# Optimization experiments

Measured on AMD Instinct MI355X. Metric: run time of the kernel, lower is better.

Reference implementation:

```python
import jax, jax.numpy as jnp
import numpy as np
import math

# ---- static configuration (mirrors init_kwargs) ----
NQ = 8            # n_qubits (main register)
NA = 2            # n_ancilla = ceil(log2(n_select))
NSEL = 4          # n_select
DEG = 3           # degree
LAYERS = 2        # n_ansatz_layers
KLOC = 2          # k_local
LATENT = 128
B = 256
NROTS = 4 * NQ * LAYERS          # 64
GROUPS = [(s, s + 1) for s in range(NQ - KLOC + 1)]  # sliding 2-local -> 7 groups
NOBS = len(GROUPS)
KDIM = 2 ** KLOC                  # 4
C64 = jnp.complex64
TWO_PI = 2.0 * math.pi

CNOT = jnp.array([[1, 0, 0, 0], [0, 1, 0, 0], [0, 0, 0, 1], [0, 0, 1, 0]], dtype=C64)

# ---- gate matrices (theta may be traced) ----
def ry_mat(th):
    c = jnp.cos(th / 2).astype(C64); s = jnp.sin(th / 2).astype(C64)
    return jnp.stack([jnp.stack([c, -s]), jnp.stack([s, c])])

def rz_mat(th):
    return jnp.diag(jnp.stack([jnp.exp(-0.5j * th), jnp.exp(0.5j * th)])).astype(C64)

def crx_mat(th):
    c = jnp.cos(th / 2).astype(C64); isn = (-1j * jnp.sin(th / 2)).astype(C64)
    one = jnp.ones((), C64)
    m = jnp.zeros((4, 4), C64)
    m = m.at[0, 0].set(one).at[1, 1].set(one)
    m = m.at[2, 2].set(c).at[3, 3].set(c).at[2, 3].set(isn).at[3, 2].set(isn)
    return m

# ---- state-vector gate application (state: (2,)*rank, wire = axis) ----
def apply_1q(state, U, w):
    return jnp.moveaxis(jnp.tensordot(U, state, axes=((1,), (w,))), 0, w)

def apply_2q(state, U, w0, w1):
    st = jnp.tensordot(U.reshape(2, 2, 2, 2), state, axes=((2, 3), (w0, w1)))
    return jnp.moveaxis(st, (0, 1), (w0, w1))

def _sim14_ops(nq, layers):
    ops, idx = [], 0
    for _ in range(layers):
        for i in range(nq):
            ops.append(("ry", (i,), idx)); idx += 1
        for i in range(nq - 1, -1, -1):
            ops.append(("crx", (i, (i + 1) % nq), idx)); idx += 1
        for i in range(nq):
            ops.append(("ry", (i,), idx)); idx += 1
        for i in [nq - 1] + list(range(nq - 1)):
            ops.append(("crx", (i, (i - 1) % nq), idx)); idx += 1
    return ops

def apply_sim14(state, p, layers, adjoint=False):
    ops = _sim14_ops(NQ, layers)
    seq = list(reversed(ops)) if adjoint else ops
    sgn = -1.0 if adjoint else 1.0
    for kind, ws, idx in seq:
        th = sgn * p[idx]
        if kind == "ry":
            state = apply_1q(state, ry_mat(th), ws[0])
        else:
            state = apply_2q(state, crx_mat(th), ws[0], ws[1])
    return state

def pcphase(state, phi):
    # e^{+i phi} on ancilla=|0..0> subspace (first 2^NQ states in (anc, main) ordering), e^{-i phi} elsewhere
    sr = state.reshape(2 ** NQ, 2 ** NA)
    ph = jnp.where(jnp.arange(2 ** NA) == 0, jnp.exp(1j * phi), jnp.exp(-1j * phi)).astype(C64)
    return (sr * ph[None, :]).reshape(state.shape)

def prepare(state, prep_p, adjoint=False):
    if not adjoint:
        for ly in range(NA):          # n_prep_layers == n_ancilla
            for qi in range(NA):
                state = apply_1q(state, ry_mat(prep_p[ly, qi, 0]), NQ + qi)
                state = apply_1q(state, rz_mat(prep_p[ly, qi, 1]), NQ + qi)
            for i in range(NA - 1):
                state = apply_2q(state, CNOT, NQ + i, NQ + i + 1)
    else:
        for ly in reversed(range(NA)):
            for i in reversed(range(NA - 1)):
                state = apply_2q(state, CNOT, NQ + i, NQ + i + 1)
            for qi in reversed(range(NA)):
                state = apply_1q(state, rz_mat(-prep_p[ly, qi, 1]), NQ + qi)
                state = apply_1q(state, ry_mat(-prep_p[ly, qi, 0]), NQ + qi)
    return state

def select(state, ts, adjoint=False):
    # ancilla wires (NQ, NQ+1) are the trailing axes; flattened index == control value s
    sr = state.reshape((2,) * NQ + (2 ** NA,))
    for s in range(NSEL):
        sub = apply_sim14(sr[..., s], ts[s], LAYERS, adjoint=adjoint)
        sr = sr.at[..., s].set(sub)
    return sr.reshape(state.shape)

def create_hermitian(A, Bp, D, N):
    h = jnp.zeros((N, N), C64)
    count = 0
    for i in range(1, N):
        h = h.at[i - 1, i - 1].set(D[i].astype(C64))
        for j in range(i):
            h = h.at[i, j].set((A[count + j] + 1j * Bp[count + j]).astype(C64))
        count += i
    return h + h.conj().T

def simulate(ts, prep_p, sig, qff, H_all):
    # ts: (NSEL, NROTS) for one batch element
    state = jnp.zeros((2,) * (NQ + NA), C64).at[(0,) * (NQ + NA)].set(1.0)
    state = pcphase(state, sig[0])
    for k in range(DEG):
        state = prepare(state, prep_p)
        state = select(state, ts, adjoint=(k % 2 == 1))
        state = prepare(state, prep_p, adjoint=True)
        state = pcphase(state, sig[k + 1])
    state = apply_sim14(state, qff, 1)
    es = []
    for w, (a, b) in enumerate(GROUPS):
        hpsi = apply_2q(state, H_all[w], a, b)
        es.append(jnp.real(jnp.vdot(state, hpsi)))
    return jnp.stack(es).astype(jnp.float32)  # (NOBS,)

def linear(x, w, b):
    return x @ w.T + b

def sinusoidal_embedding(t, dim):
    half = dim // 2
    freqs = jnp.exp(-math.log(10000.0) * jnp.arange(half, dtype=jnp.float32) / half)
    args = t[:, None] * freqs[None]
    return jnp.concatenate([jnp.cos(args), jnp.sin(args)], axis=-1)

def _forward(z_t, t, te_w1, te_b1, te_w2, te_b2, ip_w1, ip_b1, ip_w2, ip_b2,
             prep_params, signal_angles, qff_params, A_obs, B_obs, D_obs, head_w, head_b):
    t_emb = sinusoidal_embedding(t, LATENT)
    t_emb = linear(jax.nn.silu(linear(t_emb, te_w1, te_b1)), te_w2, te_b2)
    h = jnp.concatenate([z_t, t_emb], axis=-1)
    h = linear(jax.nn.silu(linear(h, ip_w1, ip_b1)), ip_w2, ip_b2)
    ts = jax.nn.sigmoid(h).reshape(z_t.shape[0], NSEL, NROTS) * TWO_PI
    H_all = jax.vmap(lambda a, b, d: create_hermitian(a, b, d, KDIM))(A_obs, B_obs, D_obs)  # (NOBS,4,4)
    expvals = jax.vmap(simulate, in_axes=(0, None, None, None, None))(
        ts, prep_params, signal_angles, qff_params, H_all)  # (B, NOBS)
    return linear(expvals, head_w, head_b)  # (B, LATENT)

def setup_inputs() -> dict:
    key = jax.random.key(0)
    ks = jax.random.split(key, 16)
    def n(k, shape, s=0.05):
        return s * jax.random.normal(k, shape, jnp.float32)
    return {
        "z_t": jax.random.normal(ks[0], (B, LATENT), jnp.float32),
        "t": jax.random.uniform(ks[1], (B,), jnp.float32),
        "te_w1": n(ks[2], (LATENT, LATENT)), "te_b1": jnp.zeros((LATENT,), jnp.float32),
        "te_w2": n(ks[3], (LATENT, LATENT)), "te_b2": jnp.zeros((LATENT,), jnp.float32),
        "ip_w1": n(ks[4], (2 * LATENT, 2 * LATENT)), "ip_b1": jnp.zeros((2 * LATENT,), jnp.float32),
        "ip_w2": n(ks[5], (NSEL * NROTS, 2 * LATENT)), "ip_b2": jnp.zeros((NSEL * NROTS,), jnp.float32),
        "prep_params": 0.1 * jax.random.normal(ks[6], (NA, NA, 2), jnp.float32),
        "signal_angles": 0.1 * jax.random.normal(ks[7], (DEG + 1,), jnp.float32),
        "qff_params": jax.random.uniform(ks[8], (4 * NQ,), jnp.float32),
        "A_obs": 2.0 * jax.random.normal(ks[9], (NOBS, KDIM * (KDIM - 1) // 2), jnp.float32),
        "B_obs": 2.0 * jax.random.normal(ks[10], (NOBS, KDIM * (KDIM - 1) // 2), jnp.float32),
        "D_obs": 2.0 * jax.random.normal(ks[11], (NOBS, KDIM), jnp.float32),
        "head_w": n(ks[12], (LATENT, NOBS)), "head_b": jnp.zeros((LATENT,), jnp.float32),
    }

def reference(z_t, t, te_w1, te_b1, te_w2, te_b2, ip_w1, ip_b1, ip_w2, ip_b2,
              prep_params, signal_angles, qff_params, A_obs, B_obs, D_obs, head_w, head_b):
    return _forward(z_t, t, te_w1, te_b1, te_w2, te_b2, ip_w1, ip_b1, ip_w2, ip_b2,
                    prep_params, signal_angles, qff_params, A_obs, B_obs, D_obs, head_w, head_b)
```

## Files before the change

### kernel.cpp

```cpp
#include <hip/hip_runtime.h>
#include <math.h>

#define NOBS 7
#define PI_F 3.14159265358979f


template<int LM>
__device__ __forceinline__ float lane_partner(float x) {
  if constexpr (LM == 1) {
    return __int_as_float(__builtin_amdgcn_mov_dpp(__float_as_int(x), 0xB1, 0xF, 0xF, true));
  } else if constexpr (LM == 2) {
    return __int_as_float(__builtin_amdgcn_mov_dpp(__float_as_int(x), 0x4E, 0xF, 0xF, true));
  } else if constexpr (LM == 4) {
    int a = __builtin_amdgcn_mov_dpp(__float_as_int(x), 0x1B, 0xF, 0xF, true);
    return __int_as_float(__builtin_amdgcn_mov_dpp(a, 0x141, 0xF, 0xF, true));
  } else if constexpr (LM == 8) {
    int a = __builtin_amdgcn_mov_dpp(__float_as_int(x), 0x141, 0xF, 0xF, true);
    return __int_as_float(__builtin_amdgcn_mov_dpp(a, 0x140, 0xF, 0xF, true));
  } else if constexpr (LM == 16) {
#if __has_builtin(__builtin_amdgcn_permlane16_swap)
    unsigned xu = __float_as_uint(x);
    auto r = __builtin_amdgcn_permlane16_swap(xu, xu, false, false);
    return (__uint_as_float(r[0]) + __uint_as_float(r[1])) - x;
#else
// ... 35 lines not shown

__device__ __forceinline__ float rdlane(float v, int idx) {
  return __int_as_float(__builtin_amdgcn_readlane(__float_as_int(v), idx));
}

__device__ __forceinline__ float2 cmul(float2 a, float2 b) {
  return make_float2(a.x*b.x - a.y*b.y, a.x*b.y + a.y*b.x);
}
__device__ __forceinline__ float2 cmulc(float2 a, float2 b) {
  return make_float2(a.x*b.x + a.y*b.y, a.y*b.x - a.x*b.y);
}
__device__ __forceinline__ float2 cadd(float2 a, float2 b) {
  return make_float2(a.x + b.x, a.y + b.y);
}

struct Ctx {
  float4* xw;
  int pp;
  int wv, lane, h;
};

__device__ __forceinline__ float4 wexch(Ctx& cx, const float* vr, const float* vi) {
  float4* buf = cx.xw + cx.pp * 512;
  buf[cx.wv * 64 + cx.lane] = make_float4(vr[0], vr[1], vi[0], vi[1]);
  __syncthreads();
  float4 p = buf[(cx.wv ^ 4) * 64 + cx.lane];
  cx.pp ^= 1;
  return p;
}


template<int W>
__device__ __forceinline__ void ry_lane(float* vr, float* vi, Ctx& cx,
                                        float ct, float st, int idx, float sg) {
  float c = rdlane(ct, idx), s = sg * rdlane(st, idx);
  constexpr int LM = 1 << (5 - W);
  const float ls = (cx.lane & LM) ? s : -s;
#pragma unroll
  for (int r = 0; r < 2; ++r) {
    float pr = lane_partner<LM>(vr[r]);
    float pi = lane_partner<LM>(vi[r]);
    vr[r] = c*vr[r] + ls*pr;
    vi[r] = c*vi[r] + ls*pi;
  }
}

__device__ __forceinline__ void ry_wave6(float* vr, float* vi, Ctx& cx,
                                         float ct, float st, int idx, float sg) {
  float c = rdlane(ct, idx), s = sg * rdlane(st, idx);
  float4 P = wexch(cx, vr, vi);
  const float ls = cx.h ? s : -s;
  vr[0] = c*vr[0] + ls*P.x;  vr[1] = c*vr[1] + ls*P.y;
  vi[0] = c*vi[0] + ls*P.z;  vi[1] = c*vi[1] + ls*P.w;
}

__device__ __forceinline__ void ry_reg7(float* vr, float* vi,
                                        float ct, float st, int idx, float sg) {
  float c = rdlane(ct, idx), s = sg * rdlane(st, idx);
  float a0 = vr[0], a1 = vr[1];
  vr[0] = c*a0 - s*a1;  vr[1] = s*a0 + c*a1;
  float b0 = vi[0], b1 = vi[1];
  vi[0] = c*b0 - s*b1;  vi[1] = s*b0 + c*b1;
}

template<int C, int T>
__device__ __forceinline__ void crx_ll(float* vr, float* vi, Ctx& cx,
                                       float ct, float st, int idx, float sg) {
  float c = rdlane(ct, idx), s = sg * rdlane(st, idx);
  constexpr int LC = 1 << (5 - C), LT = 1 << (5 - T);
  const bool act = (cx.lane & LC) != 0;
  const float cp = act ? c : 1.f, sp = act ? s : 0.f;
#pragma unroll
  for (int r = 0; r < 2; ++r) {
    float pr = lane_partner<LT>(vr[r]);
    float pi = lane_partner<LT>(vi[r]);
    vr[r] = cp*vr[r] + sp*pi;
    vi[r] = cp*vi[r] - sp*pr;
  }
}

template<int T>
__device__ __forceinline__ void crx_7l(float* vr, float* vi, Ctx& cx,
                                       float ct, float st, int idx, float sg) {
  float c = rdlane(ct, idx), s = sg * rdlane(st, idx);
  constexpr int LT = 1 << (5 - T);
  float pr = lane_partner<LT>(vr[1]);
  float pi = lane_partner<LT>(vi[1]);
  vr[1] = c*vr[1] + s*pi;
  vi[1] = c*vi[1] - s*pr;
}

template<int C>
__device__ __forceinline__ void crx_l7(float* vr, float* vi, Ctx& cx,
                                       float ct, float st, int idx, float sg) {
  float c = rdlane(ct, idx), s = sg * rdlane(st, idx);
  constexpr int LC = 1 << (5 - C);
  const bool act = (cx.lane & LC) != 0;
  const float cp = act ? c : 1.f, sp = act ? s : 0.f;
  float xr = vr[0], xi = vi[0], yr = vr[1], yi = vi[1];
  vr[0] = cp*xr + sp*yi;  vi[0] = cp*xi - sp*yr;
  vr[1] = cp*yr + sp*xi;  vi[1] = cp*yi - sp*xr;
}

template<int C>
__device__ __forceinline__ void crx_l6(float* vr, float* vi, Ctx& cx,
                                       float ct, float st, int idx, float sg) {
  float c = rdlane(ct, idx), s = sg * rdlane(st, idx);
  float4 P = wexch(cx, vr, vi);
  constexpr int LC = 1 << (5 - C);
  const bool act = (cx.lane & LC) != 0;
  const float cp = act ? c : 1.f, sp = act ? s : 0.f;
  vr[0] = cp*vr[0] + sp*P.z;  vi[0] = cp*vi[0] - sp*P.x;
  vr[1] = cp*vr[1] + sp*P.w;  vi[1] = cp*vi[1] - sp*P.y;
}

__device__ __forceinline__ void crx_76(float* vr, float* vi, Ctx& cx,
                                       float ct, float st, int idx, float sg) {
  float c = rdlane(ct, idx), s = sg * rdlane(st, idx);
  float4 P = wexch(cx, vr, vi);
  vr[1] = c*vr[1] + s*P.w;
  vi[1] = c*vi[1] - s*P.y;
}

__device__ __forceinline__ void crx_67(float* vr, float* vi, Ctx& cx,
                                       float ct, float st, int idx, float sg) {
  if (cx.h) {
    float c = rdlane(ct, idx), s = sg * rdlane(st, idx);
    float xr = vr[0], xi = vi[0], yr = vr[1], yi = vi[1];
    vr[0] = c*xr + s*yi;  vi[0] = c*xi - s*yr;
    vr[1] = c*yr + s*xi;  vi[1] = c*yi - s*xr;
  }
}

template<int T>
__device__ __forceinline__ void crx_6l(float* vr, float* vi, Ctx& cx,
                                       float ct, float st, int idx, float sg) {
  if (cx.h) {
    float c = rdlane(ct, idx), s = sg * rdlane(st, idx);
    constexpr int LT = 1 << (5 - T);
#pragma unroll
    for (int r = 0; r < 2; ++r) {
      float pr = lane_partner<LT>(vr[r]);
      float pi = lane_partner<LT>(vi[r]);
      vr[r] = c*vr[r] + s*pi;
      vi[r] = c*vi[r] - s*pr;
    }
  }
}


__device__ __forceinline__ void sim14_fwd(float* vr, float* vi, Ctx& cx,
                                          float ct, float st, int off, float sg) {
  ry_lane<0>(vr,vi,cx,ct,st,off+0,sg); ry_lane<1>(vr,vi,cx,ct,st,off+1,sg);
  ry_lane<2>(vr,vi,cx,ct,st,off+2,sg); ry_lane<3>(vr,vi,cx,ct,st,off+3,sg);
  ry_lane<4>(vr,vi,cx,ct,st,off+4,sg); ry_lane<5>(vr,vi,cx,ct,st,off+5,sg);
  ry_wave6(vr,vi,cx,ct,st,off+6,sg);   ry_reg7(vr,vi,ct,st,off+7,sg);
  crx_7l<0>(vr,vi,cx,ct,st,off+8,sg);  crx_67(vr,vi,cx,ct,st,off+9,sg);
  crx_l6<5>(vr,vi,cx,ct,st,off+10,sg); crx_ll<4,5>(vr,vi,cx,ct,st,off+11,sg);
  crx_ll<3,4>(vr,vi,cx,ct,st,off+12,sg); crx_ll<2,3>(vr,vi,cx,ct,st,off+13,sg);
  crx_ll<1,2>(vr,vi,cx,ct,st,off+14,sg); crx_ll<0,1>(vr,vi,cx,ct,st,off+15,sg);
  ry_lane<0>(vr,vi,cx,ct,st,off+16,sg); ry_lane<1>(vr,vi,cx,ct,st,off+17,sg);
  ry_lane<2>(vr,vi,cx,ct,st,off+18,sg); ry_lane<3>(vr,vi,cx,ct,st,off+19,sg);
  ry_lane<4>(vr,vi,cx,ct,st,off+20,sg); ry_lane<5>(vr,vi,cx,ct,st,off+21,sg);
  ry_wave6(vr,vi,cx,ct,st,off+22,sg);   ry_reg7(vr,vi,ct,st,off+23,sg);
  crx_76(vr,vi,cx,ct,st,off+24,sg);     crx_l7<0>(vr,vi,cx,ct,st,off+25,sg);
  crx_ll<1,0>(vr,vi,cx,ct,st,off+26,sg); crx_ll<2,1>(vr,vi,cx,ct,st,off+27,sg);
  crx_ll<3,2>(vr,vi,cx,ct,st,off+28,sg); crx_ll<4,3>(vr,vi,cx,ct,st,off+29,sg);
  crx_ll<5,4>(vr,vi,cx,ct,st,off+30,sg); crx_6l<5>(vr,vi,cx,ct,st,off+31,sg);
}

__device__ __forceinline__ void sim14_adj(float* vr, float* vi, Ctx& cx,
                                          float ct, float st, int off) {
  const float sg = -1.f;
  crx_6l<5>(vr,vi,cx,ct,st,off+31,sg); crx_ll<5,4>(vr,vi,cx,ct,st,off+30,sg);
  crx_ll<4,3>(vr,vi,cx,ct,st,off+29,sg); crx_ll<3,2>(vr,vi,cx,ct,st,off+28,sg);
  crx_ll<2,1>(vr,vi,cx,ct,st,off+27,sg); crx_ll<1,0>(vr,vi,cx,ct,st,off+26,sg);
  crx_l7<0>(vr,vi,cx,ct,st,off+25,sg);   crx_76(vr,vi,cx,ct,st,off+24,sg);
  ry_reg7(vr,vi,ct,st,off+23,sg);        ry_wave6(vr,vi,cx,ct,st,off+22,sg);
  ry_lane<5>(vr,vi,cx,ct,st,off+21,sg); ry_lane<4>(vr,vi,cx,ct,st,off+20,sg);
  ry_lane<3>(vr,vi,cx,ct,st,off+19,sg); ry_lane<2>(vr,vi,cx,ct,st,off+18,sg);
  ry_lane<1>(vr,vi,cx,ct,st,off+17,sg); ry_lane<0>(vr,vi,cx,ct,st,off+16,sg);
  crx_ll<0,1>(vr,vi,cx,ct,st,off+15,sg); crx_ll<1,2>(vr,vi,cx,ct,st,off+14,sg);
  crx_ll<2,3>(vr,vi,cx,ct,st,off+13,sg); crx_ll<3,4>(vr,vi,cx,ct,st,off+12,sg);
  crx_ll<4,5>(vr,vi,cx,ct,st,off+11,sg); crx_l6<5>(vr,vi,cx,ct,st,off+10,sg);
  crx_67(vr,vi,cx,ct,st,off+9,sg);       crx_7l<0>(vr,vi,cx,ct,st,off+8,sg);
  ry_reg7(vr,vi,ct,st,off+7,sg);         ry_wave6(vr,vi,cx,ct,st,off+6,sg);
  ry_lane<5>(vr,vi,cx,ct,st,off+5,sg); ry_lane<4>(vr,vi,cx,ct,st,off+4,sg);
  ry_lane<3>(vr,vi,cx,ct,st,off+3,sg); ry_lane<2>(vr,vi,cx,ct,st,off+2,sg);
  ry_lane<1>(vr,vi,cx,ct,st,off+1,sg); ry_lane<0>(vr,vi,cx,ct,st,off+0,sg);
}


template<int IN, int NP, int MODE>
__device__ __forceinline__ void mlp_layer(const float* __restrict__ W,
    const float* __restrict__ bias, const float* xl, float* yl,
    int rbase, int lane)
{
  const int sub = lane & 7;
  const int g   = lane >> 3;
#pragma unroll
  for (int p = 0; p < NP; ++p) {
    const int row = rbase + p * 8 + g;
    const float4* w4 = (const float4*)(W + row * IN) + sub;
    const float4* x4 = (const float4*)xl + sub;
// ... 17 lines not shown
        float sn, cn;
        __sincosf(th, &sn, &cn);
        ((float2*)yl)[row] = make_float2(cn, sn);
      }
    }
  }
}


__global__ __launch_bounds__(512) void qsvt_kernel(
    const float* __restrict__ z_t, const float* __restrict__ t,
    const float* __restrict__ te_w1, const float* __restrict__ te_b1,
    const float* __restrict__ te_w2, const float* __restrict__ te_b2,
    const float* __restrict__ ip_w1, const float* __restrict__ ip_b1,
    const float* __restrict__ ip_w2, const float* __restrict__ ip_b2,
    const float* __restrict__ prep_p, const float* __restrict__ sig,
    const float* __restrict__ qff, const float* __restrict__ A_obs,
    const float* __restrict__ B_obs, const float* __restrict__ D_obs,
    const float* __restrict__ head_w, const float* __restrict__ head_b,
    float* __restrict__ out)
{
  __shared__ __align__(16) float emb[128];
  __shared__ __align__(16) float y1[128];
  __shared__ __align__(16) float hbuf[256];
  __shared__ __align__(16) float h1[256];
  __shared__ __align__(16) float2 seltab[256];
  __shared__ __align__(16) float2 qtab[32];
  __shared__ __align__(16) float4 xw[2 * 8 * 64];
  __shared__ __align__(16) float2 xanc[128 * 9];
  __shared__ __align__(16) float dumpR[4][256];
  __shared__ __align__(16) float dumpI[4][256];
  __shared__ float redbuf[NOBS][4];
  __shared__ float hdc[NOBS][3], hxc[NOBS][6], hyc[NOBS][6];
  __shared__ __align__(16) float shw[128 * NOBS];
  __shared__ __align__(16) float shb[128];

  const int tid  = threadIdx.x;
  const int lane = tid & 63;
  const int wv   = tid >> 6;
  const int s    = wv & 3;
  const int h    = wv >> 2;
  const int b    = blockIdx.x;

  if (tid < 128) {
    int j = tid & 63;
    float fr = __expf(-9.210340371976184f * (float)j / 64.f);
    float arg = t[b] * fr;
    float sn, cn;
    __sincosf(arg, &sn, &cn);
    emb[tid] = (tid < 64) ? cn : sn;
  } else if (tid < 160) {
    int j = tid - 128;
    float sn, cn;
    __sincosf(0.5f * qff[j], &sn, &cn);
    qtab[j] = make_float2(cn, sn);
  }
  __syncthreads();

  mlp_layer<128, 2, 0>(te_w1, te_b1, emb, y1, wv * 16, lane);
  if (tid < 128) hbuf[tid] = z_t[b * 128 + tid];
  __syncthreads();

  mlp_layer<128, 2, 1>(te_w2, te_b2, y1, hbuf + 128, wv * 16, lane);
  __syncthreads();

  mlp_layer<256, 4, 0>(ip_w1, ip_b1, hbuf, h1, wv * 32, lane);
  __syncthreads();

  mlp_layer<256, 4, 2>(ip_w2, ip_b2, h1, (float*)seltab, wv * 32, lane);

  if (tid < NOBS * 6)      { hxc[tid/6][tid%6] = A_obs[tid]; hyc[tid/6][tid%6] = B_obs[tid]; }
  else if (tid >= 64 && tid < 64 + NOBS*3) { int q = tid - 64; hdc[q/3][q%3] = 2.f * D_obs[(q/3)*4 + (q%3) + 1]; }
#pragma unroll
  for (int i = tid; i < 128*NOBS; i += 512) shw[i] = head_w[i];
  if (tid < 128) shb[tid] = head_b[tid];

  float2 Ga[2][2][2], Gb[2][2][2];
#pragma unroll
  for (int ly = 0; ly < 2; ++ly) {
#pragma unroll
    for (int qi = 0; qi < 2; ++qi) {
      float y = prep_p[ly*4 + qi*2 + 0], z = prep_p[ly*4 + qi*2 + 1];
      float cy, sy, cz, sz;
      __sincosf(0.5f*y, &sy, &cy);
      __sincosf(0.5f*z, &sz, &cz);
      float2 g00 = make_float2( cy*cz, -cy*sz);
      float2 g01 = make_float2(-sy*cz,  sy*sz);
      float2 g10 = make_float2( sy*cz,  sy*sz);
      float2 g11 = make_float2( cy*cz,  cy*sz);
      if (qi == 0) { Ga[ly][0][0]=g00; Ga[ly][0][1]=g01; Ga[ly][1][0]=g10; Ga[ly][1][1]=g11; }
      else         { Gb[ly][0][0]=g00; Gb[ly][0][1]=g01; Gb[ly][1][0]=g10; Gb[ly][1][1]=g11; }
    }
  }
  float2 M[2][4][4];
#pragma unroll
  for (int ly = 0; ly < 2; ++ly) {
    float2 T[4][4];
#pragma unroll
    for (int i = 0; i < 4; ++i)
#pragma unroll
      for (int j = 0; j < 4; ++j)
        T[i][j] = cmul(Ga[ly][i>>1][j>>1], Gb[ly][i&1][j&1]);
#pragma unroll
    for (int j = 0; j < 4; ++j) {
      M[ly][0][j] = T[0][j]; M[ly][1][j] = T[1][j];
      M[ly][2][j] = T[3][j]; M[ly][3][j] = T[2][j];
    }
  }
  float2 U[4][4];
#pragma unroll
  for (int i = 0; i < 4; ++i)
#pragma unroll
    for (int j = 0; j < 4; ++j) {
      float2 acc = make_float2(0.f, 0.f);
#pragma unroll
      for (int kk = 0; kk < 4; ++kk) acc = cadd(acc, cmul(M[1][i][kk], M[0][kk][j]));
      U[i][j] = acc;
    }
  float2 Urow[4], Ucol[4];
#pragma unroll
  for (int j = 0; j < 4; ++j) {
    Urow[j] = s==0 ? U[0][j] : s==1 ? U[1][j] : s==2 ? U[2][j] : U[3][j];
    Ucol[j] = s==0 ? U[j][0] : s==1 ? U[j][1] : s==2 ? U[j][2] : U[j][3];
  }
  float sg0 = sig[0], sg1 = sig[1], sg2 = sig[2], sg3 = sig[3];
  float c1, s1v, c2, s2v, c3, s3v;
  __sincosf(sg1, &s1v, &c1);
  __sincosf(sg2, &s2v, &c2);
  __sincosf(sg3, &s3v, &c3);
  float2 R1[4], R2[4], RF[4];
  {
    float s3s = (s == 0) ? s3v : -s3v;
    float2 d3 = make_float2(c3, s3s);
#pragma unroll
    for (int sp = 0; sp < 4; ++sp) {
      float2 a1 = make_float2(0.f, 0.f), a2 = make_float2(0.f, 0.f);
#pragma unroll
      for (int j = 0; j < 4; ++j) {
        float2 uspj = sp==0 ? U[0][j] : sp==1 ? U[1][j] : sp==2 ? U[2][j] : U[3][j];
        float2 tt = cmulc(Urow[j], uspj);
        float sj = (j == 0) ? 1.f : -1.f;
        a1 = cadd(a1, cmul(tt, make_float2(c1, sj*s1v)));
        a2 = cadd(a2, cmul(tt, make_float2(c2, sj*s2v)));
      }
      R1[sp] = a1; R2[sp] = a2;
      RF[sp] = cmul(d3, make_float2(Ucol[sp].x, -Ucol[sp].y));
    }
  }
  __syncthreads();

  float2 mycs = seltab[(s << 6) | lane];
  float selc = mycs.x, sels = mycs.y;
  float2 myq = qtab[lane & 31];
  float qc = myq.x, qs = myq.y;

  Ctx cx; cx.xw = xw; cx.pp = 0; cx.wv = wv; cx.lane = lane; cx.h = h;

  float vr[2], vi[2];
  vr[0] = 0.f; vr[1] = 0.f; vi[0] = 0.f; vi[1] = 0.f;
  if (lane == 0 && h == 0) {
    float s0n, c0n;
    __sincosf(sg0, &s0n, &c0n);
    float2 a0 = cmul(Urow[0], make_float2(c0n, s0n));
    vr[0] = a0.x; vi[0] = a0.y;
  }

  const int ancbase = (h * 64 + lane) * 9;

  sim14_fwd(vr, vi, cx, selc, sels, 0, 1.f);
  sim14_fwd(vr, vi, cx, selc, sels, 32, 1.f);
  {
#pragma unroll
    for (int r = 0; r < 2; ++r) xanc[ancbase + r*4 + s] = make_float2(vr[r], vi[r]);
    __syncthreads();
#pragma unroll
    for (int r = 0; r < 2; ++r) {
      const float2* p = &xanc[ancbase + r*4];
      float2 o = cmul(R1[0], p[0]);
      o = cadd(o, cmul(R1[1], p[1]));
      o = cadd(o, cmul(R1[2], p[2]));
      o = cadd(o, cmul(R1[3], p[3]));
      vr[r] = o.x; vi[r] = o.y;
    }
    __syncthreads();
  }
  sim14_adj(vr, vi, cx, selc, sels, 32);
  sim14_adj(vr, vi, cx, selc, sels, 0);
  {
#pragma unroll
    for (int r = 0; r < 2; ++r) xanc[ancbase + r*4 + s] = make_float2(vr[r], vi[r]);
    __syncthreads();
#pragma unroll
    for (int r = 0; r < 2; ++r) {
      const float2* p = &xanc[ancbase + r*4];
      float2 o = cmul(R2[0], p[0]);
      o = cadd(o, cmul(R2[1], p[1]));
      o = cadd(o, cmul(R2[2], p[2]));
      o = cadd(o, cmul(R2[3], p[3]));
      vr[r] = o.x; vi[r] = o.y;
    }
    __syncthreads();
  }
  sim14_fwd(vr, vi, cx, selc, sels, 0, 1.f);
  sim14_fwd(vr, vi, cx, selc, sels, 32, 1.f);
  {
#pragma unroll
    for (int r = 0; r < 2; ++r) xanc[ancbase + r*4 + s] = make_float2(vr[r], vi[r]);
    __syncthreads();
#pragma unroll
    for (int r = 0; r < 2; ++r) {
      const float2* p = &xanc[ancbase + r*4];
      float2 o = cmul(RF[0], p[0]);
      o = cadd(o, cmul(RF[1], p[1]));
      o = cadd(o, cmul(RF[2], p[2]));
      o = cadd(o, cmul(RF[3], p[3]));
      vr[r] = o.x; vi[r] = o.y;
    }
    __syncthreads();
  }
  sim14_fwd(vr, vi, cx, qc, qs, 0, 1.f);

  *(float2*)&dumpR[s][(lane << 2) | (h << 1)] = make_float2(vr[0], vr[1]);
  *(float2*)&dumpI[s][(lane << 2) | (h << 1)] = make_float2(vi[0], vi[1]);
  __syncthreads();

  const int w0 = h ? 4 : 0, w1 = h ? NOBS : 4;
  for (int w = w0; w < w1; ++w) {
    const int pb = 6 - w;
    int g = lane;
    int ib = ((g >> pb) << (pb + 2)) | (g & ((1 << pb) - 1));
    float xr[4], xi[4];
#pragma unroll
    for (int i = 0; i < 4; ++i) { xr[i] = dumpR[s][ib + (i << pb)]; xi[i] = dumpI[s][ib + (i << pb)]; }
    float a = hdc[w][0] * (xr[0]*xr[0] + xi[0]*xi[0])
            + hdc[w][1] * (xr[1]*xr[1] + xi[1]*xi[1])
            + hdc[w][2] * (xr[2]*xr[2] + xi[2]*xi[2]);
    const int oi[6] = {1, 2, 2, 3, 3, 3};
    const int oj[6] = {0, 0, 1, 0, 1, 2};
// ... 16 lines not shown

  if (tid < 128) {
    float acc = shb[tid];
#pragma unroll
    for (int w = 0; w < NOBS; ++w) {
      float ev = redbuf[w][0] + redbuf[w][1] + redbuf[w][2] + redbuf[w][3];
      acc += ev * shw[tid*NOBS + w];
    }
    out[b * 128 + tid] = acc;
  }
}

extern "C" void kernel_launch(void* const* d_in, const int* in_sizes, int n_in,
                              void* d_out, int out_size, void* d_ws, size_t ws_size,
                              hipStream_t stream) {
  (void)n_in; (void)out_size; (void)d_ws; (void)ws_size;
  const float* z_t    = (const float*)d_in[0];
  const float* t      = (const float*)d_in[1];
  const float* te_w1  = (const float*)d_in[2];
  const float* te_b1  = (const float*)d_in[3];
  const float* te_w2  = (const float*)d_in[4];
  const float* te_b2  = (const float*)d_in[5];
  const float* ip_w1  = (const float*)d_in[6];
  const float* ip_b1  = (const float*)d_in[7];
  const float* ip_w2  = (const float*)d_in[8];
  const float* ip_b2  = (const float*)d_in[9];
  const float* prep_p = (const float*)d_in[10];
  const float* sig    = (const float*)d_in[11];
  const float* qff    = (const float*)d_in[12];
  const float* A_obs  = (const float*)d_in[13];
  const float* B_obs  = (const float*)d_in[14];
  const float* D_obs  = (const float*)d_in[15];
  const float* head_w = (const float*)d_in[16];
  const float* head_b = (const float*)d_in[17];
  float* out = (float*)d_out;

  int B = in_sizes[1];
  qsvt_kernel<<<B, 512, 0, stream>>>(
      z_t, t, te_w1, te_b1, te_w2, te_b2, ip_w1, ip_b1, ip_w2, ip_b2,
      prep_p, sig, qff, A_obs, B_obs, D_obs, head_w, head_b, out);
}
```

Baseline: 127.2 us.

## Precompute batch-invariant QSVT tables in setup kernel and outline sim14 circuits

Adds a one-block setup kernel that computes the ancilla prep unitary, the signal-rotation reflection matrices, the QFF cos/sin table and the timestep frequency table once, instead of redoing them in every block. The main kernel reads these from workspace and drops the per-thread register arrays R1/R2/RF. The sim14 forward and adjoint circuits become noinline functions with a dynamic shared exchange buffer, which shrinks code size and register pressure. The cost is a second kernel launch plus real function calls and global reads of the tables.

```diff
diff --git a/kernel.cpp b/kernel.cpp
--- a/kernel.cpp
+++ b/kernel.cpp
@@ -73,28 +73,24 @@
   return make_float2(a.x + b.x, a.y + b.y);
 }
 
-struct Ctx {
-  float4* xw;
-  int pp;
-  int wv, lane, h;
-};
-
-__device__ __forceinline__ float4 wexch(Ctx& cx, const float* vr, const float* vi) {
-  float4* buf = cx.xw + cx.pp * 512;
-  buf[cx.wv * 64 + cx.lane] = make_float4(vr[0], vr[1], vi[0], vi[1]);
-  __syncthreads();
-  float4 p = buf[(cx.wv ^ 4) * 64 + cx.lane];
-  cx.pp ^= 1;
-  return p;
+struct S4 { float r0, r1, i0, i1; };
+
+__device__ __forceinline__ float4 wexch(int pp, int wv, int lane,
+                                        const float* vr, const float* vi) {
+  extern __shared__ float4 dxw[];
+  float4* buf = dxw + pp * 512;
+  buf[wv * 64 + lane] = make_float4(vr[0], vr[1], vi[0], vi[1]);
+  __syncthreads();
+  return buf[(wv ^ 4) * 64 + lane];
 }
 
 
 template<int W>
-__device__ __forceinline__ void ry_lane(float* vr, float* vi, Ctx& cx,
-                                        float ct, float st, int idx, float sg) {
+__device__ __forceinline__ void ry_lane_g(float* vr, float* vi, int lane,
+                                          float ct, float st, int idx, float sg) {
   float c = rdlane(ct, idx), s = sg * rdlane(st, idx);
   constexpr int LM = 1 << (5 - W);
-  const float ls = (cx.lane & LM) ? s : -s;
+  const float ls = (lane & LM) ? s : -s;
 #pragma unroll
   for (int r = 0; r < 2; ++r) {
     float pr = lane_partner<LM>(vr[r]);
@@ -104,17 +100,17 @@
   }
 }
 
-__device__ __forceinline__ void ry_wave6(float* vr, float* vi, Ctx& cx,
-                                         float ct, float st, int idx, float sg) {
-  float c = rdlane(ct, idx), s = sg * rdlane(st, idx);
-  float4 P = wexch(cx, vr, vi);
-  const float ls = cx.h ? s : -s;
+__device__ __forceinline__ void ry_wave6_g(float* vr, float* vi, int wv, int lane, int h,
+                                           float ct, float st, int idx, float sg, int pp) {
+  float c = rdlane(ct, idx), s = sg * rdlane(st, idx);
+  float4 P = wexch(pp, wv, lane, vr, vi);
+  const float ls = h ? s : -s;
   vr[0] = c*vr[0] + ls*P.x;  vr[1] = c*vr[1] + ls*P.y;
   vi[0] = c*vi[0] + ls*P.z;  vi[1] = c*vi[1] + ls*P.w;
 }
 
-__device__ __forceinline__ void ry_reg7(float* vr, float* vi,
-                                        float ct, float st, int idx, float sg) {
+__device__ __forceinline__ void ry_reg7_g(float* vr, float* vi,
+                                          float ct, float st, int idx, float sg) {
   float c = rdlane(ct, idx), s = sg * rdlane(st, idx);
   float a0 = vr[0], a1 = vr[1];
   vr[0] = c*a0 - s*a1;  vr[1] = s*a0 + c*a1;
@@ -123,11 +119,11 @@
 }
 
 template<int C, int T>
-__device__ __forceinline__ void crx_ll(float* vr, float* vi, Ctx& cx,
-                                       float ct, float st, int idx, float sg) {
+__device__ __forceinline__ void crx_ll_g(float* vr, float* vi, int lane,
+                                         float ct, float st, int idx, float sg) {
   float c = rdlane(ct, idx), s = sg * rdlane(st, idx);
   constexpr int LC = 1 << (5 - C), LT = 1 << (5 - T);
-  const bool act = (cx.lane & LC) != 0;
+  const bool act = (lane & LC) != 0;
   const float cp = act ? c : 1.f, sp = act ? s : 0.f;
 #pragma unroll
   for (int r = 0; r < 2; ++r) {
@@ -139,8 +135,8 @@
 }
 
 template<int T>
-__device__ __forceinline__ void crx_7l(float* vr, float* vi, Ctx& cx,
-                                       float ct, float st, int idx, float sg) {
+__device__ __forceinline__ void crx_7l_g(float* vr, float* vi,
+                                         float ct, float st, int idx, float sg) {
   float c = rdlane(ct, idx), s = sg * rdlane(st, idx);
   constexpr int LT = 1 << (5 - T);
   float pr = lane_partner<LT>(vr[1]);
@@ -150,11 +146,11 @@
 }
 
 template<int C>
-__device__ __forceinline__ void crx_l7(float* vr, float* vi, Ctx& cx,
-                                       float ct, float st, int idx, float sg) {
+__device__ __forceinline__ void crx_l7_g(float* vr, float* vi, int lane,
+                                         float ct, float st, int idx, float sg) {
   float c = rdlane(ct, idx), s = sg * rdlane(st, idx);
   constexpr int LC = 1 << (5 - C);
-  const bool act = (cx.lane & LC) != 0;
+  const bool act = (lane & LC) != 0;
   const float cp = act ? c : 1.f, sp = act ? s : 0.f;
   float xr = vr[0], xi = vi[0], yr = vr[1], yi = vi[1];
   vr[0] = cp*xr + sp*yi;  vi[0] = cp*xi - sp*yr;
@@ -162,28 +158,28 @@
 }
 
 template<int C>
-__device__ __forceinline__ void crx_l6(float* vr, float* vi, Ctx& cx,
-                                       float ct, float st, int idx, float sg) {
-  float c = rdlane(ct, idx), s = sg * rdlane(st, idx);
-  float4 P = wexch(cx, vr, vi);
+__device__ __forceinline__ void crx_l6_g(float* vr, float* vi, int wv, int lane,
+                                         float ct, float st, int idx, float sg, int pp) {
+  float c = rdlane(ct, idx), s = sg * rdlane(st, idx);
+  float4 P = wexch(pp, wv, lane, vr, vi);
   constexpr int LC = 1 << (5 - C);
-  const bool act = (cx.lane & LC) != 0;
+  const bool act = (lane & LC) != 0;
   const float cp = act ? c : 1.f, sp = act ? s : 0.f;
   vr[0] = cp*vr[0] + sp*P.z;  vi[0] = cp*vi[0] - sp*P.x;
   vr[1] = cp*vr[1] + sp*P.w;  vi[1] = cp*vi[1] - sp*P.y;
 }
 
-__device__ __forceinline__ void crx_76(float* vr, float* vi, Ctx& cx,
-                                       float ct, float st, int idx, float sg) {
-  float c = rdlane(ct, idx), s = sg * rdlane(st, idx);
-  float4 P = wexch(cx, vr, vi);
+__device__ __forceinline__ void crx_76_g(float* vr, float* vi, int wv, int lane,
+                                         float ct, float st, int idx, float sg, int pp) {
+  float c = rdlane(ct, idx), s = sg * rdlane(st, idx);
+  float4 P = wexch(pp, wv, lane, vr, vi);
   vr[1] = c*vr[1] + s*P.w;
   vi[1] = c*vi[1] - s*P.y;
 }
 
-__device__ __forceinline__ void crx_67(float* vr, float* vi, Ctx& cx,
-                                       float ct, float st, int idx, float sg) {
-  if (cx.h) {
+__device__ __forceinline__ void crx_67_g(float* vr, float* vi, int h,
+                                         float ct, float st, int idx, float sg) {
+  if (h) {
     float c = rdlane(ct, idx), s = sg * rdlane(st, idx);
     float xr = vr[0], xi = vi[0], yr = vr[1], yi = vi[1];
     vr[0] = c*xr + s*yi;  vi[0] = c*xi - s*yr;
@@ -192,9 +188,9 @@
 }
 
 template<int T>
-__device__ __forceinline__ void crx_6l(float* vr, float* vi, Ctx& cx,
-                                       float ct, float st, int idx, float sg) {
-  if (cx.h) {
+__device__ __forceinline__ void crx_6l_g(float* vr, float* vi, int h,
+                                         float ct, float st, int idx, float sg) {
+  if (h) {
     float c = rdlane(ct, idx), s = sg * rdlane(st, idx);
     constexpr int LT = 1 << (5 - T);
 #pragma unroll
@@ -208,45 +204,133 @@
 }
 
 
-__device__ __forceinline__ void sim14_fwd(float* vr, float* vi, Ctx& cx,
-                                          float ct, float st, int off, float sg) {
-  ry_lane<0>(vr,vi,cx,ct,st,off+0,sg); ry_lane<1>(vr,vi,cx,ct,st,off+1,sg);
-  ry_lane<2>(vr,vi,cx,ct,st,off+2,sg); ry_lane<3>(vr,vi,cx,ct,st,off+3,sg);
-  ry_lane<4>(vr,vi,cx,ct,st,off+4,sg); ry_lane<5>(vr,vi,cx,ct,st,off+5,sg);
-  ry_wave6(vr,vi,cx,ct,st,off+6,sg);   ry_reg7(vr,vi,ct,st,off+7,sg);
-  crx_7l<0>(vr,vi,cx,ct,st,off+8,sg);  crx_67(vr,vi,cx,ct,st,off+9,sg);
-  crx_l6<5>(vr,vi,cx,ct,st,off+10,sg); crx_ll<4,5>(vr,vi,cx,ct,st,off+11,sg);
-  crx_ll<3,4>(vr,vi,cx,ct,st,off+12,sg); crx_ll<2,3>(vr,vi,cx,ct,st,off+13,sg);
-  crx_ll<1,2>(vr,vi,cx,ct,st,off+14,sg); crx_ll<0,1>(vr,vi,cx,ct,st,off+15,sg);
-  ry_lane<0>(vr,vi,cx,ct,st,off+16,sg); ry_lane<1>(vr,vi,cx,ct,st,off+17,sg);
-  ry_lane<2>(vr,vi,cx,ct,st,off+18,sg); ry_lane<3>(vr,vi,cx,ct,st,off+19,sg);
-  ry_lane<4>(vr,vi,cx,ct,st,off+20,sg); ry_lane<5>(vr,vi,cx,ct,st,off+21,sg);
-  ry_wave6(vr,vi,cx,ct,st,off+22,sg);   ry_reg7(vr,vi,ct,st,off+23,sg);
-  crx_76(vr,vi,cx,ct,st,off+24,sg);     crx_l7<0>(vr,vi,cx,ct,st,off+25,sg);
-  crx_ll<1,0>(vr,vi,cx,ct,st,off+26,sg); crx_ll<2,1>(vr,vi,cx,ct,st,off+27,sg);
-  crx_ll<3,2>(vr,vi,cx,ct,st,off+28,sg); crx_ll<4,3>(vr,vi,cx,ct,st,off+29,sg);
-  crx_ll<5,4>(vr,vi,cx,ct,st,off+30,sg); crx_6l<5>(vr,vi,cx,ct,st,off+31,sg);
-}
-
-__device__ __forceinline__ void sim14_adj(float* vr, float* vi, Ctx& cx,
-                                          float ct, float st, int off) {
+__device__ __noinline__ S4 sim14_fwd(S4 v, float ct, float st, int off) {
+  const int tid = threadIdx.x;
+  const int lane = tid & 63, wv = tid >> 6, h = wv >> 2;
+  float vr[2] = {v.r0, v.r1}, vi[2] = {v.i0, v.i1};
+  const float sg = 1.f;
+  ry_lane_g<0>(vr,vi,lane,ct,st,off+0,sg); ry_lane_g<1>(vr,vi,lane,ct,st,off+1,sg);
+  ry_lane_g<2>(vr,vi,lane,ct,st,off+2,sg); ry_lane_g<3>(vr,vi,lane,ct,st,off+3,sg);
+  ry_lane_g<4>(vr,vi,lane,ct,st,off+4,sg); ry_lane_g<5>(vr,vi,lane,ct,st,off+5,sg);
+  ry_wave6_g(vr,vi,wv,lane,h,ct,st,off+6,sg,0);
+  ry_reg7_g(vr,vi,ct,st,off+7,sg);
+  crx_7l_g<0>(vr,vi,ct,st,off+8,sg);
+  crx_67_g(vr,vi,h,ct,st,off+9,sg);
+  crx_l6_g<5>(vr,vi,wv,lane,ct,st,off+10,sg,1);
+  crx_ll_g<4,5>(vr,vi,lane,ct,st,off+11,sg); crx_ll_g<3,4>(vr,vi,lane,ct,st,off+12,sg);
+  crx_ll_g<2,3>(vr,vi,lane,ct,st,off+13,sg); crx_ll_g<1,2>(vr,vi,lane,ct,st,off+14,sg);
+  crx_ll_g<0,1>(vr,vi,lane,ct,st,off+15,sg);
+  ry_lane_g<0>(vr,vi,lane,ct,st,off+16,sg); ry_lane_g<1>(vr,vi,lane,ct,st,off+17,sg);
+  ry_lane_g<2>(vr,vi,lane,ct,st,off+18,sg); ry_lane_g<3>(vr,vi,lane,ct,st,off+19,sg);
+  ry_lane_g<4>(vr,vi,lane,ct,st,off+20,sg); ry_lane_g<5>(vr,vi,lane,ct,st,off+21,sg);
+  ry_wave6_g(vr,vi,wv,lane,h,ct,st,off+22,sg,0);
+  ry_reg7_g(vr,vi,ct,st,off+23,sg);
+  crx_76_g(vr,vi,wv,lane,ct,st,off+24,sg,1);
+  crx_l7_g<0>(vr,vi,lane,ct,st,off+25,sg);
+  crx_ll_g<1,0>(vr,vi,lane,ct,st,off+26,sg); crx_ll_g<2,1>(vr,vi,lane,ct,st,off+27,sg);
+  crx_ll_g<3,2>(vr,vi,lane,ct,st,off+28,sg); crx_ll_g<4,3>(vr,vi,lane,ct,st,off+29,sg);
+  crx_ll_g<5,4>(vr,vi,lane,ct,st,off+30,sg);
+  crx_6l_g<5>(vr,vi,h,ct,st,off+31,sg);
+  return {vr[0], vr[1], vi[0], vi[1]};
+}
+
+__device__ __noinline__ S4 sim14_adj(S4 v, float ct, float st, int off) {
+  const int tid = threadIdx.x;
+  const int lane = tid & 63, wv = tid >> 6, h = wv >> 2;
+  float vr[2] = {v.r0, v.r1}, vi[2] = {v.i0, v.i1};
   const float sg = -1.f;
-  crx_6l<5>(vr,vi,cx,ct,st,off+31,sg); crx_ll<5,4>(vr,vi,cx,ct,st,off+30,sg);
-  crx_ll<4,3>(vr,vi,cx,ct,st,off+29,sg); crx_ll<3,2>(vr,vi,cx,ct,st,off+28,sg);
-  crx_ll<2,1>(vr,vi,cx,ct,st,off+27,sg); crx_ll<1,0>(vr,vi,cx,ct,st,off+26,sg);
-  crx_l7<0>(vr,vi,cx,ct,st,off+25,sg);   crx_76(vr,vi,cx,ct,st,off+24,sg);
-  ry_reg7(vr,vi,ct,st,off+23,sg);        ry_wave6(vr,vi,cx,ct,st,off+22,sg);
-  ry_lane<5>(vr,vi,cx,ct,st,off+21,sg); ry_lane<4>(vr,vi,cx,ct,st,off+20,sg);
-  ry_lane<3>(vr,vi,cx,ct,st,off+19,sg); ry_lane<2>(vr,vi,cx,ct,st,off+18,sg);
-  ry_lane<1>(vr,vi,cx,ct,st,off+17,sg); ry_lane<0>(vr,vi,cx,ct,st,off+16,sg);
-  crx_ll<0,1>(vr,vi,cx,ct,st,off+15,sg); crx_ll<1,2>(vr,vi,cx,ct,st,off+14,sg);
-  crx_ll<2,3>(vr,vi,cx,ct,st,off+13,sg); crx_ll<3,4>(vr,vi,cx,ct,st,off+12,sg);
-  crx_ll<4,5>(vr,vi,cx,ct,st,off+11,sg); crx_l6<5>(vr,vi,cx,ct,st,off+10,sg);
-  crx_67(vr,vi,cx,ct,st,off+9,sg);       crx_7l<0>(vr,vi,cx,ct,st,off+8,sg);
-  ry_reg7(vr,vi,ct,st,off+7,sg);         ry_wave6(vr,vi,cx,ct,st,off+6,sg);
-  ry_lane<5>(vr,vi,cx,ct,st,off+5,sg); ry_lane<4>(vr,vi,cx,ct,st,off+4,sg);
-  ry_lane<3>(vr,vi,cx,ct,st,off+3,sg); ry_lane<2>(vr,vi,cx,ct,st,off+2,sg);
-  ry_lane<1>(vr,vi,cx,ct,st,off+1,sg); ry_lane<0>(vr,vi,cx,ct,st,off+0,sg);
+  crx_6l_g<5>(vr,vi,h,ct,st,off+31,sg);
+  crx_ll_g<5,4>(vr,vi,lane,ct,st,off+30,sg); crx_ll_g<4,3>(vr,vi,lane,ct,st,off+29,sg);
+  crx_ll_g<3,2>(vr,vi,lane,ct,st,off+28,sg); crx_ll_g<2,1>(vr,vi,lane,ct,st,off+27,sg);
+  crx_ll_g<1,0>(vr,vi,lane,ct,st,off+26,sg);
+  crx_l7_g<0>(vr,vi,lane,ct,st,off+25,sg);
+  crx_76_g(vr,vi,wv,lane,ct,st,off+24,sg,0);
+  ry_reg7_g(vr,vi,ct,st,off+23,sg);
+  ry_wave6_g(vr,vi,wv,lane,h,ct,st,off+22,sg,1);
+  ry_lane_g<5>(vr,vi,lane,ct,st,off+21,sg); ry_lane_g<4>(vr,vi,lane,ct,st,off+20,sg);
+  ry_lane_g<3>(vr,vi,lane,ct,st,off+19,sg); ry_lane_g<2>(vr,vi,lane,ct,st,off+18,sg);
+  ry_lane_g<1>(vr,vi,lane,ct,st,off+17,sg); ry_lane_g<0>(vr,vi,lane,ct,st,off+16,sg);
+  crx_ll_g<0,1>(vr,vi,lane,ct,st,off+15,sg); crx_ll_g<1,2>(vr,vi,lane,ct,st,off+14,sg);
+  crx_ll_g<2,3>(vr,vi,lane,ct,st,off+13,sg); crx_ll_g<3,4>(vr,vi,lane,ct,st,off+12,sg);
+  crx_ll_g<4,5>(vr,vi,lane,ct,st,off+11,sg);
+  crx_l6_g<5>(vr,vi,wv,lane,ct,st,off+10,sg,0);
+  crx_67_g(vr,vi,h,ct,st,off+9,sg);
+  crx_7l_g<0>(vr,vi,ct,st,off+8,sg);
+  ry_reg7_g(vr,vi,ct,st,off+7,sg);
+  ry_wave6_g(vr,vi,wv,lane,h,ct,st,off+6,sg,1);
+  ry_lane_g<5>(vr,vi,lane,ct,st,off+5,sg); ry_lane_g<4>(vr,vi,lane,ct,st,off+4,sg);
+  ry_lane_g<3>(vr,vi,lane,ct,st,off+3,sg); ry_lane_g<2>(vr,vi,lane,ct,st,off+2,sg);
+  ry_lane_g<1>(vr,vi,lane,ct,st,off+1,sg); ry_lane_g<0>(vr,vi,lane,ct,st,off+0,sg);
+  return {vr[0], vr[1], vi[0], vi[1]};
+}
+
+
+__global__ void setup_kernel(const float* __restrict__ prep_p,
+                             const float* __restrict__ sig,
+                             const float* __restrict__ qff,
+                             float* __restrict__ ws) {
+  const int t = threadIdx.x;
+  float2 Ga[2][2][2], Gb[2][2][2];
+  for (int ly = 0; ly < 2; ++ly)
+    for (int qi = 0; qi < 2; ++qi) {
+      float y = prep_p[ly*4 + qi*2 + 0], z = prep_p[ly*4 + qi*2 + 1];
+      float cy, sy, cz, sz;
+      __sincosf(0.5f*y, &sy, &cy);
+      __sincosf(0.5f*z, &sz, &cz);
+      float2 g00 = make_float2( cy*cz, -cy*sz);
+      float2 g01 = make_float2(-sy*cz,  sy*sz);
+      float2 g10 = make_float2( sy*cz,  sy*sz);
+      float2 g11 = make_float2( cy*cz,  cy*sz);
+      if (qi == 0) { Ga[ly][0][0]=g00; Ga[ly][0][1]=g01; Ga[ly][1][0]=g10; Ga[ly][1][1]=g11; }
+      else         { Gb[ly][0][0]=g00; Gb[ly][0][1]=g01; Gb[ly][1][0]=g10; Gb[ly][1][1]=g11; }
+    }
+  float2 M[2][4][4];
+  for (int ly = 0; ly < 2; ++ly) {
+    float2 T[4][4];
+    for (int i = 0; i < 4; ++i)
+      for (int j = 0; j < 4; ++j)
+        T[i][j] = cmul(Ga[ly][i>>1][j>>1], Gb[ly][i&1][j&1]);
+    for (int j = 0; j < 4; ++j) {
+      M[ly][0][j] = T[0][j]; M[ly][1][j] = T[1][j];
+      M[ly][2][j] = T[3][j]; M[ly][3][j] = T[2][j];
+    }
+  }
+  float2 U[4][4];
+  for (int i = 0; i < 4; ++i)
+    for (int j = 0; j < 4; ++j) {
+      float2 acc = make_float2(0.f, 0.f);
+      for (int kk = 0; kk < 4; ++kk) acc = cadd(acc, cmul(M[1][i][kk], M[0][kk][j]));
+      U[i][j] = acc;
+    }
+  float c0n, s0n, c1, s1v, c2, s2v, c3, s3v;
+  __sincosf(sig[0], &s0n, &c0n);
+  __sincosf(sig[1], &s1v, &c1);
+  __sincosf(sig[2], &s2v, &c2);
+  __sincosf(sig[3], &s3v, &c3);
+
+  if (t < 16) {
+    int i = t >> 2, j = t & 3;
+    float2 a1 = make_float2(0.f, 0.f), a2 = make_float2(0.f, 0.f);
+    for (int k = 0; k < 4; ++k) {
+      float2 tt = cmulc(U[i][k], U[j][k]);
+      float sk = (k == 0) ? 1.f : -1.f;
+      a1 = cadd(a1, cmul(tt, make_float2(c1, sk*s1v)));
+      a2 = cadd(a2, cmul(tt, make_float2(c2, sk*s2v)));
+    }
+    ((float2*)ws)[t]        = a1;
+    ((float2*)(ws + 32))[t] = a2;
+    float2 d3 = make_float2(c3, (i == 0) ? s3v : -s3v);
+    ((float2*)(ws + 64))[t] = cmul(d3, make_float2(U[j][i].x, -U[j][i].y));
+  }
+  if (t < 4) {
+    ((float2*)(ws + 96))[t] = cmul(U[t][0], make_float2(c0n, s0n));
+  }
+  if (t < 32) {
+    float sn, cn;
+    __sincosf(0.5f * qff[t], &sn, &cn);
+    ((float2*)(ws + 104))[t] = make_float2(cn, sn);
+  }
+  ws[168 + t] = __expf(-9.210340371976184f * (float)t / 64.f);
 }
 
 
@@ -294,10 +378,10 @@
     const float* __restrict__ te_w2, const float* __restrict__ te_b2,
     const float* __restrict__ ip_w1, const float* __restrict__ ip_b1,
     const float* __restrict__ ip_w2, const float* __restrict__ ip_b2,
-    const float* __restrict__ prep_p, const float* __restrict__ sig,
-    const float* __restrict__ qff, const float* __restrict__ A_obs,
-    const float* __restrict__ B_obs, const float* __restrict__ D_obs,
+    const float* __restrict__ A_obs, const float* __restrict__ B_obs,
+    const float* __restrict__ D_obs,
     const float* __restrict__ head_w, const float* __restrict__ head_b,
+    const float* __restrict__ ws,
     float* __restrict__ out)
 {
   __shared__ __align__(16) float emb[128];
@@ -305,8 +389,6 @@
   __shared__ __align__(16) float hbuf[256];
   __shared__ __align__(16) float h1[256];
   __shared__ __align__(16) float2 seltab[256];
-  __shared__ __align__(16) float2 qtab[32];
-  __shared__ __align__(16) float4 xw[2 * 8 * 64];
   __shared__ __align__(16) float2 xanc[128 * 9];
   __shared__ __align__(16) float dumpR[4][256];
   __shared__ __align__(16) float dumpI[4][256];
@@ -323,17 +405,11 @@
   const int b    = blockIdx.x;
 
   if (tid < 128) {
-    int j = tid & 63;
-    float fr = __expf(-9.210340371976184f * (float)j / 64.f);
+    float fr = ws[168 + (tid & 63)];
     float arg = t[b] * fr;
     float sn, cn;
     __sincosf(arg, &sn, &cn);
     emb[tid] = (tid < 64) ? cn : sn;
-  } else if (tid < 160) {
-    int j = tid - 128;
-    float sn, cn;
-    __sincosf(0.5f * qff[j], &sn, &cn);
-    qtab[j] = make_float2(cn, sn);
   }
   __syncthreads();
 
@@ -354,154 +430,80 @@
 #pragma unroll
   for (int i = tid; i < 128*NOBS; i += 512) shw[i] = head_w[i];
   if (tid < 128) shb[tid] = head_b[tid];
-
-  float2 Ga[2][2][2], Gb[2][2][2];
-#pragma unroll
-  for (int ly = 0; ly < 2; ++ly) {
-#pragma unroll
-    for (int qi = 0; qi < 2; ++qi) {
-      float y = prep_p[ly*4 + qi*2 + 0], z = prep_p[ly*4 + qi*2 + 1];
-      float cy, sy, cz, sz;
-      __sincosf(0.5f*y, &sy, &cy);
-      __sincosf(0.5f*z, &sz, &cz);
-      float2 g00 = make_float2( cy*cz, -cy*sz);
-      float2 g01 = make_float2(-sy*cz,  sy*sz);
-      float2 g10 = make_float2( sy*cz,  sy*sz);
-      float2 g11 = make_float2( cy*cz,  cy*sz);
-      if (qi == 0) { Ga[ly][0][0]=g00; Ga[ly][0][1]=g01; Ga[ly][1][0]=g10; Ga[ly][1][1]=g11; }
-      else         { Gb[ly][0][0]=g00; Gb[ly][0][1]=g01; Gb[ly][1][0]=g10; Gb[ly][1][1]=g11; }
-    }
-  }
-  float2 M[2][4][4];
-#pragma unroll
-  for (int ly = 0; ly < 2; ++ly) {
-    float2 T[4][4];
-#pragma unroll
-    for (int i = 0; i < 4; ++i)
-#pragma unroll
-      for (int j = 0; j < 4; ++j)
-        T[i][j] = cmul(Ga[ly][i>>1][j>>1], Gb[ly][i&1][j&1]);
-#pragma unroll
-    for (int j = 0; j < 4; ++j) {
-      M[ly][0][j] = T[0][j]; M[ly][1][j] = T[1][j];
-      M[ly][2][j] = T[3][j]; M[ly][3][j] = T[2][j];
-    }
-  }
-  float2 U[4][4];
-#pragma unroll
-  for (int i = 0; i < 4; ++i)
-#pragma unroll
-    for (int j = 0; j < 4; ++j) {
-      float2 acc = make_float2(0.f, 0.f);
-#pragma unroll
-      for (int kk = 0; kk < 4; ++kk) acc = cadd(acc, cmul(M[1][i][kk], M[0][kk][j]));
-      U[i][j] = acc;
-    }
-  float2 Urow[4], Ucol[4];
-#pragma unroll
-  for (int j = 0; j < 4; ++j) {
-    Urow[j] = s==0 ? U[0][j] : s==1 ? U[1][j] : s==2 ? U[2][j] : U[3][j];
-    Ucol[j] = s==0 ? U[j][0] : s==1 ? U[j][1] : s==2 ? U[j][2] : U[j][3];
-  }
-  float sg0 = sig[0], sg1 = sig[1], sg2 = sig[2], sg3 = sig[3];
-  float c1, s1v, c2, s2v, c3, s3v;
-  __sincosf(sg1, &s1v, &c1);
-  __sincosf(sg2, &s2v, &c2);
-  __sincosf(sg3, &s3v, &c3);
-  float2 R1[4], R2[4], RF[4];
-  {
-    float s3s = (s == 0) ? s3v : -s3v;
-    float2 d3 = make_float2(c3, s3s);
-#pragma unroll
-    for (int sp = 0; sp < 4; ++sp) {
-      float2 a1 = make_float2(0.f, 0.f), a2 = make_float2(0.f, 0.f);
-#pragma unroll
-      for (int j = 0; j < 4; ++j) {
-        float2 uspj = sp==0 ? U[0][j] : sp==1 ? U[1][j] : sp==2 ? U[2][j] : U[3][j];
-        float2 tt = cmulc(Urow[j], uspj);
-        float sj = (j == 0) ? 1.f : -1.f;
-        a1 = cadd(a1, cmul(tt, make_float2(c1, sj*s1v)));
-        a2 = cadd(a2, cmul(tt, make_float2(c2, sj*s2v)));
-      }
-      R1[sp] = a1; R2[sp] = a2;
-      RF[sp] = cmul(d3, make_float2(Ucol[sp].x, -Ucol[sp].y));
-    }
-  }
   __syncthreads();
 
   float2 mycs = seltab[(s << 6) | lane];
   float selc = mycs.x, sels = mycs.y;
-  float2 myq = qtab[lane & 31];
+  float2 myq = ((const float2*)(ws + 104))[lane & 31];
   float qc = myq.x, qs = myq.y;
 
-  Ctx cx; cx.xw = xw; cx.pp = 0; cx.wv = wv; cx.lane = lane; cx.h = h;
-
-  float vr[2], vi[2];
-  vr[0] = 0.f; vr[1] = 0.f; vi[0] = 0.f; vi[1] = 0.f;
+  S4 v;
+  v.r0 = 0.f; v.r1 = 0.f; v.i0 = 0.f; v.i1 = 0.f;
   if (lane == 0 && h == 0) {
-    float s0n, c0n;
-    __sincosf(sg0, &s0n, &c0n);
-    float2 a0 = cmul(Urow[0], make_float2(c0n, s0n));
-    vr[0] = a0.x; vi[0] = a0.y;
+    float2 a0 = ((const float2*)(ws + 96))[s];
+    v.r0 = a0.x; v.i0 = a0.y;
   }
 
   const int ancbase = (h * 64 + lane) * 9;
 
-  sim14_fwd(vr, vi, cx, selc, sels, 0, 1.f);
-  sim14_fwd(vr, vi, cx, selc, sels, 32, 1.f);
+  v = sim14_fwd(v, selc, sels, 0);
+  v = sim14_fwd(v, selc, sels, 32);
   {
-#pragma unroll
-    for (int r = 0; r < 2; ++r) xanc[ancbase + r*4 + s] = make_float2(vr[r], vi[r]);
+    const float2* R = (const float2*)ws + (s << 2);
+    xanc[ancbase + 0 + s] = make_float2(v.r0, v.i0);
+    xanc[ancbase + 4 + s] = make_float2(v.r1, v.i1);
     __syncthreads();
-#pragma unroll
-    for (int r = 0; r < 2; ++r) {
-      const float2* p = &xanc[ancbase + r*4];
-      float2 o = cmul(R1[0], p[0]);
-      o = cadd(o, cmul(R1[1], p[1]));
-      o = cadd(o, cmul(R1[2], p[2]));
-      o = cadd(o, cmul(R1[3], p[3]));
-      vr[r] = o.x; vi[r] = o.y;
-    }
+    float2 o0 = cmul(R[0], xanc[ancbase + 0]);
+    o0 = cadd(o0, cmul(R[1], xanc[ancbase + 1]));
+    o0 = cadd(o0, cmul(R[2], xanc[ancbase + 2]));
+    o0 = cadd(o0, cmul(R[3], xanc[ancbase + 3]));
+    float2 o1 = cmul(R[0], xanc[ancbase + 4]);
+    o1 = cadd(o1, cmul(R[1], xanc[ancbase + 5]));
+    o1 = cadd(o1, cmul(R[2], xanc[ancbase + 6]));
+    o1 = cadd(o1, cmul(R[3], xanc[ancbase + 7]));
+    v.r0 = o0.x; v.i0 = o0.y; v.r1 = o1.x; v.i1 = o1.y;
     __syncthreads();
   }
-  sim14_adj(vr, vi, cx, selc, sels, 32);
-  sim14_adj(vr, vi, cx, selc, sels, 0);
+  v = sim14_adj(v, selc, sels, 32);
+  v = sim14_adj(v, selc, sels, 0);
   {
-#pragma unroll
-    for (int r = 0; r < 2; ++r) xanc[ancbase + r*4 + s] = make_float2(vr[r], vi[r]);
+    const float2* R = (const float2*)(ws + 32) + (s << 2);
+    xanc[ancbase + 0 + s] = make_float2(v.r0, v.i0);
+    xanc[ancbase + 4 + s] = make_float2(v.r1, v.i1);
     __syncthreads();
-#pragma unroll
-    for (int r = 0; r < 2; ++r) {
-      const float2* p = &xanc[ancbase + r*4];
-      float2 o = cmul(R2[0], p[0]);
-      o = cadd(o, cmul(R2[1], p[1]));
-      o = cadd(o, cmul(R2[2], p[2]));
-      o = cadd(o, cmul(R2[3], p[3]));
-      vr[r] = o.x; vi[r] = o.y;
-    }
+    float2 o0 = cmul(R[0], xanc[ancbase + 0]);
+    o0 = cadd(o0, cmul(R[1], xanc[ancbase + 1]));
+    o0 = cadd(o0, cmul(R[2], xanc[ancbase + 2]));
+    o0 = cadd(o0, cmul(R[3], xanc[ancbase + 3]));
+    float2 o1 = cmul(R[0], xanc[ancbase + 4]);
+    o1 = cadd(o1, cmul(R[1], xanc[ancbase + 5]));
+    o1 = cadd(o1, cmul(R[2], xanc[ancbase + 6]));
+    o1 = cadd(o1, cmul(R[3], xanc[ancbase + 7]));
+    v.r0 = o0.x; v.i0 = o0.y; v.r1 = o1.x; v.i1 = o1.y;
     __syncthreads();
   }
-  sim14_fwd(vr, vi, cx, selc, sels, 0, 1.f);
-  sim14_fwd(vr, vi, cx, selc, sels, 32, 1.f);
+  v = sim14_fwd(v, selc, sels, 0);
+  v = sim14_fwd(v, selc, sels, 32);
   {
-#pragma unroll
-    for (int r = 0; r < 2; ++r) xanc[ancbase + r*4 + s] = make_float2(vr[r], vi[r]);
+    const float2* R = (const float2*)(ws + 64) + (s << 2);
+    xanc[ancbase + 0 + s] = make_float2(v.r0, v.i0);
+    xanc[ancbase + 4 + s] = make_float2(v.r1, v.i1);
     __syncthreads();
-#pragma unroll
-    for (int r = 0; r < 2; ++r) {
-      const float2* p = &xanc[ancbase + r*4];
-      float2 o = cmul(RF[0], p[0]);
-      o = cadd(o, cmul(RF[1], p[1]));
-      o = cadd(o, cmul(RF[2], p[2]));
-      o = cadd(o, cmul(RF[3], p[3]));
-      vr[r] = o.x; vi[r] = o.y;
-    }
+    float2 o0 = cmul(R[0], xanc[ancbase + 0]);
+    o0 = cadd(o0, cmul(R[1], xanc[ancbase + 1]));
+    o0 = cadd(o0, cmul(R[2], xanc[ancbase + 2]));
+    o0 = cadd(o0, cmul(R[3], xanc[ancbase + 3]));
+    float2 o1 = cmul(R[0], xanc[ancbase + 4]);
+    o1 = cadd(o1, cmul(R[1], xanc[ancbase + 5]));
+    o1 = cadd(o1, cmul(R[2], xanc[ancbase + 6]));
+    o1 = cadd(o1, cmul(R[3], xanc[ancbase + 7]));
+    v.r0 = o0.x; v.i0 = o0.y; v.r1 = o1.x; v.i1 = o1.y;
     __syncthreads();
   }
-  sim14_fwd(vr, vi, cx, qc, qs, 0, 1.f);
-
-  *(float2*)&dumpR[s][(lane << 2) | (h << 1)] = make_float2(vr[0], vr[1]);
-  *(float2*)&dumpI[s][(lane << 2) | (h << 1)] = make_float2(vi[0], vi[1]);
+  v = sim14_fwd(v, qc, qs, 0);
+
+  *(float2*)&dumpR[s][(lane << 2) | (h << 1)] = make_float2(v.r0, v.r1);
+  *(float2*)&dumpI[s][(lane << 2) | (h << 1)] = make_float2(v.i0, v.i1);
   __syncthreads();
 
   const int w0 = h ? 4 : 0, w1 = h ? NOBS : 4;
@@ -548,7 +550,7 @@
 extern "C" void kernel_launch(void* const* d_in, const int* in_sizes, int n_in,
                               void* d_out, int out_size, void* d_ws, size_t ws_size,
                               hipStream_t stream) {
-  (void)n_in; (void)out_size; (void)d_ws; (void)ws_size;
+  (void)n_in; (void)out_size; (void)ws_size;
   const float* z_t    = (const float*)d_in[0];
   const float* t      = (const float*)d_in[1];
   const float* te_w1  = (const float*)d_in[2];
@@ -568,9 +570,12 @@
   const float* head_w = (const float*)d_in[16];
   const float* head_b = (const float*)d_in[17];
   float* out = (float*)d_out;
+  float* ws  = (float*)d_ws;
+
+  setup_kernel<<<1, 64, 0, stream>>>(prep_p, sig, qff, ws);
 
   int B = in_sizes[1];
-  qsvt_kernel<<<B, 512, 0, stream>>>(
+  qsvt_kernel<<<B, 512, 2 * 512 * sizeof(float4), stream>>>(
       z_t, t, te_w1, te_b1, te_w2, te_b2, ip_w1, ip_b1, ip_w2, ip_b2,
-      prep_p, sig, qff, A_obs, B_obs, D_obs, head_w, head_b, out);
-}
+      A_obs, B_obs, D_obs, head_w, head_b, ws, out);
+}
```

New measurement: 127.4 us. No clear change (+0.2%).
